# Optimization experiments

Hardware: AMD Instinct MI355X
Metric: run time of the kernel (lower is better)

The kernel has to match this reference:

```python
import jax, jax.numpy as jnp
import numpy as np

H = 8          # nhead
EPS_Z = 1e-6   # linear-attention normalizer eps
LN_EPS = 1e-5  # torch LayerNorm default


def _ln(x, g, b):
    m = x.mean(-1, keepdims=True)
    v = ((x - m) ** 2).mean(-1, keepdims=True)
    return (x - m) * jax.lax.rsqrt(v + LN_EPS) * g + b


def setup_inputs() -> dict:
    key = jax.random.key(0)
    ks = jax.random.split(key, 8)
    B, S, E, F = 4, 8192, 512, 2048
    s = 0.02
    return {
        "src": jax.random.normal(ks[0], (B, S, E), jnp.float32),
        "Wq": jax.random.normal(ks[1], (E, E), jnp.float32) * s,
        "bq": jnp.zeros((E,), jnp.float32),
        "Wk": jax.random.normal(ks[2], (E, E), jnp.float32) * s,
        "bk": jnp.zeros((E,), jnp.float32),
        "Wv": jax.random.normal(ks[3], (E, E), jnp.float32) * s,
        "bv": jnp.zeros((E,), jnp.float32),
        "Wo": jax.random.normal(ks[4], (E, E), jnp.float32) * s,
        "bo": jnp.zeros((E,), jnp.float32),
        "W1": jax.random.normal(ks[5], (E, F), jnp.float32) * s,
        "b1": jnp.zeros((F,), jnp.float32),
        "W2": jax.random.normal(ks[6], (F, E), jnp.float32) * s,
        "b2": jnp.zeros((E,), jnp.float32),
        "g1": jnp.ones((E,), jnp.float32),
        "be1": jnp.zeros((E,), jnp.float32),
        "g2": jnp.ones((E,), jnp.float32),
        "be2": jnp.zeros((E,), jnp.float32),
    }


def reference(src, Wq, bq, Wk, bk, Wv, bv, Wo, bo, W1, b1, W2, b2, g1, be1, g2, be2):
    B, S, E = src.shape
    Dh = E // H

    def heads(x):  # [B,S,E] -> [B,H,S,Dh]
        return x.reshape(B, S, H, Dh).transpose(0, 2, 1, 3)

    q = heads(src @ Wq + bq)
    k = heads(src @ Wk + bk)
    v = heads(src @ Wv + bv)

    qm = jax.nn.elu(q) + 1.0  # feature map: ELU+1
    km = jax.nn.elu(k) + 1.0

    kv = jnp.einsum("bhsd,bhse->bhde", km, v)          # [B,H,Dh,Dh]
    ksum = km.sum(axis=2)                               # [B,H,Dh]
    z = 1.0 / (jnp.einsum("bhsd,bhd->bhs", qm, ksum) + EPS_Z)
    attn = jnp.einsum("bhsd,bhde->bhse", qm, kv) * z[..., None]

    attn = attn.transpose(0, 2, 1, 3).reshape(B, S, E) @ Wo + bo
    x = _ln(src + attn, g1, be1)
    ff = jax.nn.relu(x @ W1 + b1) @ W2 + b2
    return _ln(x + ff, g2, be2)
```

## Files before the change

kernel.cpp:

```cpp
#include <hip/hip_runtime.h>
#include <hip/hip_bf16.h>

typedef __attribute__((ext_vector_type(8))) short bf16x8;
typedef __attribute__((ext_vector_type(4))) float f32x4;

__device__ inline ushort f2bf(float f) {
    uint u = __float_as_uint(f);
    u += 0x7fff + ((u >> 16) & 1);
    return (ushort)(u >> 16);
}
__device__ inline float bf2f(ushort h) {
    return __uint_as_float(((uint)h) << 16);
}

__device__ inline void gload16(const void* g, void* lds) {
    __builtin_amdgcn_global_load_lds(
        (const __attribute__((address_space(1))) void*)g,
        (__attribute__((address_space(3))) void*)lds, 16, 0, 0);
}

__global__ __launch_bounds__(256) void prep(
    const float* __restrict__ src, ushort* __restrict__ src16,
    const float* __restrict__ Wq, const float* __restrict__ Wk,
    const float* __restrict__ Wv, const float* __restrict__ Wo,
    const float* __restrict__ W1, const float* __restrict__ W2,
    ushort* __restrict__ wqkv, ushort* __restrict__ wot,
    ushort* __restrict__ w1t, ushort* __restrict__ w2t,
    const float* __restrict__ bq, const float* __restrict__ bk,
    const float* __restrict__ bv, float* __restrict__ bqkv) {
    __shared__ float tile[32][33];
    int bid = blockIdx.x;
    const int t = threadIdx.x;
    if (bid < 16384) {
        int i = bid * 256 + t;
        float4 a = ((const float4*)src)[i];
        ushort4 o;
        o.x = f2bf(a.x); o.y = f2bf(a.y); o.z = f2bf(a.z); o.w = f2bf(a.w);
        ((ushort4*)src16)[i] = o;
        return;
    }
    bid -= 16384;
    const float* in; ushort* out; int Kd, Nd;
    if (bid < 1024) {
        int m = bid >> 8;
        in = (m == 0) ? Wq : (m == 1) ? Wk : (m == 2) ? Wv : Wo;
        out = (m == 3) ? wot : (wqkv + m * 512 * 512);
        Kd = 512; Nd = 512; bid &= 255;
    } else if (bid < 2048) { in = W1; out = w1t; Kd = 512; Nd = 2048; bid -= 1024; }
    else if (bid < 3072) { in = W2; out = w2t; Kd = 2048; Nd = 512; bid -= 2048; }
    else {
        int i = (bid - 3072) * 256 + t;
        if (i < 512) bqkv[i] = bq[i];
        else if (i < 1024) bqkv[i] = bk[i - 512];
        else if (i < 1536) bqkv[i] = bv[i - 1024];
        return;
    }
    const int nx = Nd / 32;
    const int nbase = (bid % nx) * 32, kb = (bid / nx) * 32;
    const int tx = t & 31, ty = t >> 5;
#pragma unroll
    for (int i = 0; i < 4; i++)
        tile[ty + i * 8][tx] = in[(size_t)(kb + ty + i * 8) * Nd + nbase + tx];
    __syncthreads();
#pragma unroll
    for (int i = 0; i < 4; i++) {
        int n = nbase + ty + i * 8, k = kb + tx;
        out[(size_t)n * Kd + k] = f2bf(tile[tx][ty + i * 8]);
    }
}

template <int EPI, int NT, int GB>
__global__ __launch_bounds__(512, 2) void gemm256(
    const ushort* __restrict__ A, const ushort* __restrict__ Bt,
    const float* __restrict__ bias, const ushort* __restrict__ res16,
    ushort* __restrict__ out16, int M, int N, int K, int nb1) {
    extern __shared__ char smem[];
    const int t = threadIdx.x;
    const int w = t >> 6, l = t & 63;
    const int wr = w >> 2, wc = w & 3;
    const int nwg = gridDim.x;
    const int cpx = nwg >> 3;
    const int swz = (blockIdx.x & 7) * cpx + (blockIdx.x >> 3);
    int bx0, by0;
    if (GB == 0) { bx0 = (swz % nb1) * NT; by0 = swz / nb1; }
    else         { bx0 = swz % nb1;        by0 = (swz / nb1) * NT; }

    const int sc = (t & 3) ^ ((t >> 3) & 3);
    const ushort* gA0 = A + (size_t)(by0 * 256 + (t >> 2)) * K + sc * 8;
    const ushort* gA1 = gA0 + (size_t)128 * K;
    const ushort* gB0 = Bt + (size_t)(bx0 * 256 + (t >> 2)) * K + sc * 8;
    const ushort* gB1 = gB0 + (size_t)128 * K;

    const int Kt = K >> 5;
    const int TOT = NT * Kt;
    int stg_kt = 0, stg_g = 0;
    size_t stgA = 0, stgB = 0;

    auto stage_h0 = [&]() {
        char* Lb = smem + (stg_g & 3) * 32768 + (w << 10);
        gload16(gA0 + stgA + stg_kt * 32, Lb);
        gload16(gB0 + stgB + stg_kt * 32, Lb + 16384);
    };
    auto stage_h1 = [&]() {
        char* Lb = smem + (stg_g & 3) * 32768 + (w << 10);
        gload16(gA1 + stgA + stg_kt * 32, Lb + 8192);
        gload16(gB1 + stgB + stg_kt * 32, Lb + 24576);
        ++stg_g;
        if (++stg_kt == Kt) {
            stg_kt = 0;
            if (GB == 0) stgB += (size_t)256 * K;
            else         stgA += (size_t)256 * K;
        }
    };

    f32x4 acc[8][4] = {};

    const int R0a = wr * 128 + (l & 15);
    const int offA = R0a * 64 + (((l >> 4) ^ ((R0a >> 1) & 3)) << 4);
    const int R0b = wc * 64 + (l & 15);
    const int offB = 16384 + R0b * 64 + (((l >> 4) ^ ((R0b >> 1) & 3)) << 4);

    stage_h0(); stage_h1();
    stage_h0(); stage_h1();
    stage_h0(); stage_h1();

    int g = 0;
    for (int j = 0; j < NT; ++j) {
#pragma unroll 1
        for (int kt = 0; kt < Kt; ++kt, ++g) {
            const int rem = TOT - 1 - g;
            if (rem >= 2)      asm volatile("s_waitcnt vmcnt(8)" ::: "memory");
            else if (rem == 1) asm volatile("s_waitcnt vmcnt(4)" ::: "memory");
            else               asm volatile("s_waitcnt vmcnt(0)" ::: "memory");
            __builtin_amdgcn_s_barrier();
            __builtin_amdgcn_sched_barrier(0);

            const char* bufp = smem + (g & 3) * 32768;
            if (g + 3 < TOT) { stage_h0(); stage_h1(); }

            bf16x8 a[8], b[4];
#pragma unroll
            for (int n = 0; n < 4; n++) b[n] = *(const bf16x8*)(bufp + offB + n * 1024);
#pragma unroll
            for (int m = 0; m < 8; m++) a[m] = *(const bf16x8*)(bufp + offA + m * 1024);

            __builtin_amdgcn_s_setprio(1);
#pragma unroll
            for (int m = 0; m < 8; m++)
#pragma unroll
                for (int n = 0; n < 4; n++)
                    acc[m][n] = __builtin_amdgcn_mfma_f32_16x16x32_bf16(a[m], b[n], acc[m][n], 0, 0, 0);
            __builtin_amdgcn_s_setprio(0);
            __builtin_amdgcn_sched_barrier(0);
        }

        {
            const int bx = (GB == 0) ? (bx0 + j) : bx0;
            const int by = (GB == 0) ? by0 : (by0 + j);
            const int row0 = by * 256 + wr * 128 + ((l >> 4) << 2);
            const int col0 = bx * 256 + wc * 64 + (l & 15);
            const int seg = bx >> 1;
            const size_t segoff = (size_t)seg * M * 512;
            const int c511 = col0 & 511;
            float bv[4];
#pragma unroll
            for (int n = 0; n < 4; n++) bv[n] = bias[col0 + n * 16];
#pragma unroll
            for (int m = 0; m < 8; m++) {
#pragma unroll
                for (int r = 0; r < 4; r++) {
                    const int row = row0 + m * 16 + r;
                    const size_t base = (size_t)row * N + col0;
#pragma unroll
                    for (int n = 0; n < 4; n++) {
                        float vv = acc[m][n][r] + bv[n];
                        if constexpr (EPI == 2) {
                            vv = vv > 0.f ? vv : 0.f;
                            out16[base + n * 16] = f2bf(vv);
                        } else if constexpr (EPI == 3) {
                            vv += bf2f(res16[base + n * 16]);
                            out16[base + n * 16] = f2bf(vv);
                        } else if constexpr (EPI == 4) {
                            if (seg < 2) vv = vv > 0.f ? vv + 1.f : __expf(vv);
                            out16[segoff + (size_t)row * 512 + c511 + n * 16] = f2bf(vv);
                        } else {
                            out16[base + n * 16] = f2bf(vv);
                        }
                    }
                }
            }
            if (j + 1 < NT) {
#pragma unroll
                for (int m = 0; m < 8; m++)
#pragma unroll
                    for (int n = 0; n < 4; n++)
                        acc[m][n] = (f32x4){0.f, 0.f, 0.f, 0.f};
            }
        }
    }
}

__global__ __launch_bounds__(256) void kv_partial(
    const ushort* __restrict__ km, const ushort* __restrict__ v,
    float* __restrict__ kvp, float* __restrict__ ksump, int S) {
    __shared__ ushort kms[32 * 64];
    __shared__ ushort vs[32 * 64];
    const int t = threadIdx.x;
    const int bh = blockIdx.y, b = bh >> 3, h = bh & 7;
    const int d0 = (t >> 4) * 4, e0 = (t & 15) * 4;
    float acc[4][4] = {};
    float ks = 0.f;
    const int s_base = blockIdx.x * 512;
    const int r = t >> 3, c8 = (t & 7) * 8;
    for (int s0 = 0; s0 < 512; s0 += 32) {
        size_t grow = ((size_t)b * S + s_base + s0 + r) * 512 + h * 64 + c8;
        *(uint4*)&kms[r * 64 + c8] = *(const uint4*)&km[grow];
        *(uint4*)&vs[r * 64 + c8] = *(const uint4*)&v[grow];
        __syncthreads();
#pragma unroll 4
        for (int s = 0; s < 32; ++s) {
            ushort4 ka = *(const ushort4*)&kms[s * 64 + d0];
            ushort4 vb = *(const ushort4*)&vs[s * 64 + e0];
            float a0 = bf2f(ka.x), a1 = bf2f(ka.y), a2 = bf2f(ka.z), a3 = bf2f(ka.w);
            float b0 = bf2f(vb.x), b1 = bf2f(vb.y), b2 = bf2f(vb.z), b3 = bf2f(vb.w);
            acc[0][0] += a0 * b0; acc[0][1] += a0 * b1; acc[0][2] += a0 * b2; acc[0][3] += a0 * b3;
            acc[1][0] += a1 * b0; acc[1][1] += a1 * b1; acc[1][2] += a1 * b2; acc[1][3] += a1 * b3;
            acc[2][0] += a2 * b0; acc[2][1] += a2 * b1; acc[2][2] += a2 * b2; acc[2][3] += a2 * b3;
            acc[3][0] += a3 * b0; acc[3][1] += a3 * b1; acc[3][2] += a3 * b2; acc[3][3] += a3 * b3;
            if (t < 64) ks += bf2f(kms[s * 64 + t]);
        }
        __syncthreads();
    }
    float* dst = kvp + ((size_t)bh * 16 + blockIdx.x) * 4096;
#pragma unroll
    for (int i = 0; i < 4; i++)
#pragma unroll
        for (int j = 0; j < 4; j++)
            dst[(d0 + i) * 64 + e0 + j] = acc[i][j];
    if (t < 64) ksump[((size_t)bh * 16 + blockIdx.x) * 64 + t] = ks;
}

__global__ void kv_reduce(const float* __restrict__ kvp, const float* __restrict__ ksump,
                          ushort* __restrict__ kvt, float* __restrict__ ksum) {
    int i = blockIdx.x * 256 + threadIdx.x;
    if (i < 32 * 4096) {
        int bh = i >> 12, de = i & 4095;
        int d = de >> 6, e = de & 63;
        float s = 0.f;
#pragma unroll
        for (int c = 0; c < 16; ++c) s += kvp[((size_t)bh * 16 + c) * 4096 + de];
        kvt[(size_t)bh * 4096 + e * 64 + d] = f2bf(s);
    } else {
        int j = i - 32 * 4096;
        if (j < 32 * 64) {
            int bh = j >> 6, d = j & 63;
            float s = 0.f;
#pragma unroll
            for (int c = 0; c < 16; ++c) s += ksump[((size_t)bh * 16 + c) * 64 + d];
            ksum[j] = s;
        }
    }
}

__global__ __launch_bounds__(256) void attn_mfma(
    const ushort* __restrict__ qm, const ushort* __restrict__ kvt,
    const float* __restrict__ ksum, ushort* __restrict__ attnE, int S) {
    __shared__ ushort As[128 * 128];
    __shared__ ushort Bs[128 * 64];
    __shared__ float zbuf[128][2];
    __shared__ float ks2[128];
    const int t = threadIdx.x, w = t >> 6, l = t & 63;
    const int cx = blockIdx.x, by = blockIdx.y;
    const int b = (by * 128) / S;
    const int h0 = cx * 2;
    const size_t arow0 = (size_t)(by * 128) * 512 + cx * 128;

#pragma unroll
    for (int rd = 0; rd < 8; ++rd) {
        const ushort* g = qm + arow0 + (size_t)(rd * 16 + w * 4 + (l >> 4)) * 512 + (l & 15) * 8;
        gload16(g, (char*)As + rd * 4096 + w * 1024);
    }
    const ushort* kvbase = kvt + (size_t)(b * 8 + h0) * 4096;
#pragma unroll
    for (int rd = 0; rd < 4; ++rd) {
        const ushort* g = kvbase + (rd * 32 + w * 8 + (l >> 3)) * 64 + (l & 7) * 8;
        gload16(g, (char*)Bs + rd * 4096 + w * 1024);
    }
    if (t < 128) ks2[t] = ksum[(b * 8 + h0) * 64 + t];
    __syncthreads();

    {
        const int r = t >> 1, hh = t & 1;
        float den = 0.f;
#pragma unroll
        for (int d0 = 0; d0 < 64; d0 += 8) {
            bf16x8 qv = *(const bf16x8*)&As[r * 128 + hh * 64 + d0];
#pragma unroll
            for (int j = 0; j < 8; j++) den += bf2f((ushort)qv[j]) * ks2[hh * 64 + d0 + j];
        }
        zbuf[r][hh] = 1.0f / (den + 1e-6f);
    }

    const int wr = w >> 1, wc = w & 1;
    const int ar = wr * 64 + (l & 15);
    const int br = wc * 64 + (l & 15);
    const int ko = (l >> 4) * 8;
    f32x4 acc[4][4] = {};
#pragma unroll
    for (int ks_ = 0; ks_ < 2; ++ks_) {
        bf16x8 a[4], bb[4];
#pragma unroll
        for (int m = 0; m < 4; m++)
            a[m] = *(const bf16x8*)&As[(ar + m * 16) * 128 + wc * 64 + ks_ * 32 + ko];
#pragma unroll
        for (int n = 0; n < 4; n++)
            bb[n] = *(const bf16x8*)&Bs[(br + n * 16) * 64 + ks_ * 32 + ko];
#pragma unroll
        for (int m = 0; m < 4; m++)
#pragma unroll
            for (int n = 0; n < 4; n++)
                acc[m][n] = __builtin_amdgcn_mfma_f32_16x16x32_bf16(a[m], bb[n], acc[m][n], 0, 0, 0);
    }
    __syncthreads();

    const int row0l = wr * 64 + ((l >> 4) << 2);
    ushort* outbase = attnE + (size_t)(by * 128) * 512 + cx * 128;
#pragma unroll
    for (int n = 0; n < 4; n++) {
#pragma unroll
        for (int m = 0; m < 4; m++) {
#pragma unroll
            for (int r = 0; r < 4; r++) {
                int rl = row0l + m * 16 + r;
                float z = zbuf[rl][wc];
                outbase[(size_t)rl * 512 + wc * 64 + n * 16 + (l & 15)] = f2bf(acc[m][n][r] * z);
            }
        }
    }
}

template <int OUT32>
__global__ __launch_bounds__(256) void ln_bf16(
    const ushort* __restrict__ in, const float* __restrict__ g, const float* __restrict__ be,
    void* __restrict__ outp, int Mrows) {
    const int w = threadIdx.x >> 6, l = threadIdx.x & 63;
    const int row = blockIdx.x * 4 + w;
    if (row >= Mrows) return;
    const ushort* rp = in + (size_t)row * 512;
    uint4 u = *(const uint4*)&rp[l * 8];
    float x[8];
    x[0] = bf2f((ushort)(u.x & 0xffff)); x[1] = bf2f((ushort)(u.x >> 16));
    x[2] = bf2f((ushort)(u.y & 0xffff)); x[3] = bf2f((ushort)(u.y >> 16));
    x[4] = bf2f((ushort)(u.z & 0xffff)); x[5] = bf2f((ushort)(u.z >> 16));
    x[6] = bf2f((ushort)(u.w & 0xffff)); x[7] = bf2f((ushort)(u.w >> 16));
    float s = 0.f, ss = 0.f;
#pragma unroll
    for (int j = 0; j < 8; j++) { s += x[j]; ss += x[j] * x[j]; }
#pragma unroll
    for (int o = 1; o < 64; o <<= 1) {
        s += __shfl_xor(s, o, 64);
        ss += __shfl_xor(ss, o, 64);
    }
    float mean = s * (1.f / 512.f);
    float var = ss * (1.f / 512.f) - mean * mean;
    float rstd = rsqrtf(var + 1e-5f);
    float4 g0 = *(const float4*)&g[l * 8], g1v = *(const float4*)&g[l * 8 + 4];
    float4 b0 = *(const float4*)&be[l * 8], b1v = *(const float4*)&be[l * 8 + 4];
    float o0[8];
    o0[0] = (x[0] - mean) * rstd * g0.x + b0.x;
    o0[1] = (x[1] - mean) * rstd * g0.y + b0.y;
    o0[2] = (x[2] - mean) * rstd * g0.z + b0.z;
    o0[3] = (x[3] - mean) * rstd * g0.w + b0.w;
    o0[4] = (x[4] - mean) * rstd * g1v.x + b1v.x;
    o0[5] = (x[5] - mean) * rstd * g1v.y + b1v.y;
    o0[6] = (x[6] - mean) * rstd * g1v.z + b1v.z;
    o0[7] = (x[7] - mean) * rstd * g1v.w + b1v.w;
    if constexpr (OUT32) {
        float* op = (float*)outp + (size_t)row * 512;
        *(float4*)&op[l * 8] = make_float4(o0[0], o0[1], o0[2], o0[3]);
        *(float4*)&op[l * 8 + 4] = make_float4(o0[4], o0[5], o0[6], o0[7]);
    } else {
        ushort* op = (ushort*)outp + (size_t)row * 512;
        ushort4 u0, u1;
        u0.x = f2bf(o0[0]); u0.y = f2bf(o0[1]); u0.z = f2bf(o0[2]); u0.w = f2bf(o0[3]);
        u1.x = f2bf(o0[4]); u1.y = f2bf(o0[5]); u1.z = f2bf(o0[6]); u1.w = f2bf(o0[7]);
        *(ushort4*)&op[l * 8] = u0;
        *(ushort4*)&op[l * 8 + 4] = u1;
    }
}

extern "C" void kernel_launch(void* const* d_in, const int* in_sizes, int n_in,
                              void* d_out, int out_size, void* d_ws, size_t ws_size,
                              hipStream_t stream) {
    const int B = 4, S = 8192, E = 512, F = 2048;
    const int M = B * S;
    const size_t SZ = (size_t)M * E * 2;
    const int SMEM = 131072;

    const float* src = (const float*)d_in[0];
    const float* Wq = (const float*)d_in[1];  const float* bq = (const float*)d_in[2];
    const float* Wk = (const float*)d_in[3];  const float* bk = (const float*)d_in[4];
    const float* Wv = (const float*)d_in[5];  const float* bv = (const float*)d_in[6];
    const float* Wo = (const float*)d_in[7];  const float* bo = (const float*)d_in[8];
    const float* W1 = (const float*)d_in[9];  const float* b1 = (const float*)d_in[10];
    const float* W2 = (const float*)d_in[11]; const float* b2 = (const float*)d_in[12];
    const float* g1 = (const float*)d_in[13]; const float* be1 = (const float*)d_in[14];
    const float* g2 = (const float*)d_in[15]; const float* be2 = (const float*)d_in[16];

    char* ws = (char*)d_ws;
    ushort* qm    = (ushort*)(ws + 0 * SZ);
    ushort* km    = (ushort*)(ws + 1 * SZ);
    ushort* v     = (ushort*)(ws + 2 * SZ);
    ushort* src16 = (ushort*)(ws + 3 * SZ);
    ushort* x16   = (ushort*)(ws + 4 * SZ);
    ushort* z16   = (ushort*)(ws + 5 * SZ);
    char*   tail  = ws + 6 * SZ;
    float*  kvp   = (float*)(tail);
    float*  ksump = (float*)(tail + 8388608);
    ushort* kvt   = (ushort*)(tail + 8519680);
    float*  ksum  = (float*)(tail + 8781824);
    float*  bqkv  = (float*)(tail + 8790016);
    ushort* wqkv  = (ushort*)(tail + 8796160);
    ushort* wot   = (ushort*)(tail + 10369024);
    ushort* w1t   = (ushort*)(tail + 10893312);
    ushort* w2t   = (ushort*)(tail + 12990464);
    ushort* attnE = km;
    ushort* y16   = v;
    ushort* hbuf  = (ushort*)(ws + 0);

    hipFuncSetAttribute((const void*)gemm256<4, 3, 0>, hipFuncAttributeMaxDynamicSharedMemorySize, SMEM);
    hipFuncSetAttribute((const void*)gemm256<3, 1, 0>, hipFuncAttributeMaxDynamicSharedMemorySize, SMEM);
    hipFuncSetAttribute((const void*)gemm256<2, 4, 1>, hipFuncAttributeMaxDynamicSharedMemorySize, SMEM);

    prep<<<dim3(16384 + 3072 + 6), 256, 0, stream>>>(
        src, src16, Wq, Wk, Wv, Wo, W1, W2, wqkv, wot, w1t, w2t, bq, bk, bv, bqkv);

    gemm256<4, 3, 0><<<dim3(2 * 128), 512, SMEM, stream>>>(src16, wqkv, bqkv, nullptr, qm, M, 1536, E, 2);

    kv_partial<<<dim3(16, 32), 256, 0, stream>>>(km, v, kvp, ksump, S);
    kv_reduce<<<dim3((32 * 4096 + 32 * 64 + 255) / 256), 256, 0, stream>>>(kvp, ksump, kvt, ksum);

    attn_mfma<<<dim3(4, M / 128), 256, 0, stream>>>(qm, kvt, ksum, attnE, S);

    gemm256<3, 1, 0><<<dim3(2 * 128), 512, SMEM, stream>>>(attnE, wot, bo, src16, y16, M, E, E, 2);
    ln_bf16<0><<<dim3(M / 4), 256, 0, stream>>>(y16, g1, be1, x16, M);

    gemm256<2, 4, 1><<<dim3(8 * 32), 512, SMEM, stream>>>(x16, w1t, b1, nullptr, hbuf, M, F, E, 8);
    gemm256<3, 1, 0><<<dim3(2 * 128), 512, SMEM, stream>>>(hbuf, w2t, b2, x16, z16, M, E, F, 2);
    ln_bf16<1><<<dim3(M / 4), 256, 0, stream>>>(z16, g2, be2, (float*)d_out, M);
}
```

Measured before the change: 364.8 us.

## Restructure GEMM mainloop to double-buffered BK=64 with interleaved staging phases

The 256x256 bf16 GEMM drops its 4-stage BK=32 ring buffer for a 2-stage BK=64 double buffer with an 8-way XOR swizzle. Each K-step is split into four phases that interleave LDS fragment reads, global-to-LDS staging of the next tile, fine-grained vmcnt/lgkmcnt waits and MFMA groups, with barriers between phases. The goal is to halve loop overhead per K and overlap loads with compute more evenly. In exchange there are many more barriers per iteration and a shallower prefetch depth, which could expose memory latency.

```diff
diff --git a/kernel.cpp b/kernel.cpp
--- a/kernel.cpp
+++ b/kernel.cpp
@@ -78,80 +78,103 @@
     const int t = threadIdx.x;
     const int w = t >> 6, l = t & 63;
     const int wr = w >> 2, wc = w & 3;
-    const int nwg = gridDim.x;
-    const int cpx = nwg >> 3;
+    const int nwg = gridDim.x, cpx = nwg >> 3;
     const int swz = (blockIdx.x & 7) * cpx + (blockIdx.x >> 3);
     int bx0, by0;
     if (GB == 0) { bx0 = (swz % nb1) * NT; by0 = swz / nb1; }
     else         { bx0 = swz % nb1;        by0 = (swz / nb1) * NT; }
 
-    const int sc = (t & 3) ^ ((t >> 3) & 3);
-    const ushort* gA0 = A + (size_t)(by0 * 256 + (t >> 2)) * K + sc * 8;
-    const ushort* gA1 = gA0 + (size_t)128 * K;
-    const ushort* gB0 = Bt + (size_t)(bx0 * 256 + (t >> 2)) * K + sc * 8;
-    const ushort* gB1 = gB0 + (size_t)128 * K;
-
-    const int Kt = K >> 5;
+    const int scoff = ((t & 7) ^ ((t >> 3) & 7)) * 8;
+    const ushort* pA = A + (size_t)(by0 * 256 + (t >> 3)) * K + scoff;
+    const ushort* pB = Bt + (size_t)(bx0 * 256 + (t >> 3)) * K + scoff;
+    const size_t u64K = (size_t)64 * K;
+
+    const int Kt = K >> 6;
     const int TOT = NT * Kt;
-    int stg_kt = 0, stg_g = 0;
-    size_t stgA = 0, stgB = 0;
-
-    auto stage_h0 = [&]() {
-        char* Lb = smem + (stg_g & 3) * 32768 + (w << 10);
-        gload16(gA0 + stgA + stg_kt * 32, Lb);
-        gload16(gB0 + stgB + stg_kt * 32, Lb + 16384);
-    };
-    auto stage_h1 = [&]() {
-        char* Lb = smem + (stg_g & 3) * 32768 + (w << 10);
-        gload16(gA1 + stgA + stg_kt * 32, Lb + 8192);
-        gload16(gB1 + stgB + stg_kt * 32, Lb + 24576);
-        ++stg_g;
-        if (++stg_kt == Kt) {
-            stg_kt = 0;
-            if (GB == 0) stgB += (size_t)256 * K;
-            else         stgA += (size_t)256 * K;
-        }
-    };
+    int skt = 0;
+    size_t adv = 0;
+
+    const int cA0 = ((l >> 4) ^ (l & 7)) * 16;
+    const int cA1 = ((4 + (l >> 4)) ^ (l & 7)) * 16;
+    const int baseA = (wr * 128 + (l & 15)) * 128;
+    const int baseB = 32768 + (wc * 64 + (l & 15)) * 128;
+
+    char* nb = smem;
+
+#define STG(uid)                                                                        \
+    {                                                                                   \
+        char* dst = nb + ((uid) < 4 ? (uid) * 8192 : 32768 + ((uid) - 4) * 8192) + (w << 10); \
+        const ushort* s = ((uid) < 4)                                                   \
+            ? (pA + (size_t)(uid) * u64K + (GB ? adv : 0) + skt * 64)                   \
+            : (pB + (size_t)((uid) - 4) * u64K + (GB ? 0 : adv) + skt * 64);            \
+        gload16(s, dst);                                                                \
+    }
+
+    STG(4); STG(5); STG(6); STG(7); STG(0); STG(2); STG(1); STG(3);
+    if (++skt == Kt) { skt = 0; adv += (size_t)256 * K; }
+    asm volatile("s_waitcnt vmcnt(2)" ::: "memory");
+    __builtin_amdgcn_s_barrier();
 
     f32x4 acc[8][4] = {};
-
-    const int R0a = wr * 128 + (l & 15);
-    const int offA = R0a * 64 + (((l >> 4) ^ ((R0a >> 1) & 3)) << 4);
-    const int R0b = wc * 64 + (l & 15);
-    const int offB = 16384 + R0b * 64 + (((l >> 4) ^ ((R0b >> 1) & 3)) << 4);
-
-    stage_h0(); stage_h1();
-    stage_h0(); stage_h1();
-    stage_h0(); stage_h1();
-
+    bf16x8 b[4][2];
     int g = 0;
     for (int j = 0; j < NT; ++j) {
 #pragma unroll 1
         for (int kt = 0; kt < Kt; ++kt, ++g) {
-            const int rem = TOT - 1 - g;
-            if (rem >= 2)      asm volatile("s_waitcnt vmcnt(8)" ::: "memory");
-            else if (rem == 1) asm volatile("s_waitcnt vmcnt(4)" ::: "memory");
-            else               asm volatile("s_waitcnt vmcnt(0)" ::: "memory");
-            __builtin_amdgcn_s_barrier();
-            __builtin_amdgcn_sched_barrier(0);
-
-            const char* bufp = smem + (g & 3) * 32768;
-            if (g + 3 < TOT) { stage_h0(); stage_h1(); }
-
-            bf16x8 a[8], b[4];
-#pragma unroll
-            for (int n = 0; n < 4; n++) b[n] = *(const bf16x8*)(bufp + offB + n * 1024);
-#pragma unroll
-            for (int m = 0; m < 8; m++) a[m] = *(const bf16x8*)(bufp + offA + m * 1024);
-
-            __builtin_amdgcn_s_setprio(1);
-#pragma unroll
-            for (int m = 0; m < 8; m++)
-#pragma unroll
-                for (int n = 0; n < 4; n++)
-                    acc[m][n] = __builtin_amdgcn_mfma_f32_16x16x32_bf16(a[m], b[n], acc[m][n], 0, 0, 0);
-            __builtin_amdgcn_s_setprio(0);
-            __builtin_amdgcn_sched_barrier(0);
+            const char* cb = smem + (g & 1) * 65536;
+            nb = smem + ((g + 1) & 1) * 65536;
+            const bool ds = (g + 1 < TOT);
+#pragma unroll
+            for (int p = 0; p < 4; ++p) {
+                bf16x8 af[2][2];
+                if (p == 0) {
+#pragma unroll
+                    for (int n = 0; n < 4; n++) {
+                        b[n][0] = *(const bf16x8*)(cb + baseB + n * 2048 + cA0);
+                        b[n][1] = *(const bf16x8*)(cb + baseB + n * 2048 + cA1);
+                    }
+                }
+                af[0][0] = *(const bf16x8*)(cb + baseA + (2 * p) * 2048 + cA0);
+                af[0][1] = *(const bf16x8*)(cb + baseA + (2 * p) * 2048 + cA1);
+                af[1][0] = *(const bf16x8*)(cb + baseA + (2 * p + 1) * 2048 + cA0);
+                af[1][1] = *(const bf16x8*)(cb + baseA + (2 * p + 1) * 2048 + cA1);
+                if (ds) {
+                    if (p == 0)      { STG(4); STG(5); }
+                    else if (p == 1) { STG(6); STG(7); }
+                    else if (p == 2) { STG(0); STG(2); }
+                    else             { STG(1); STG(3); }
+                }
+                if (p == 0) asm volatile("s_waitcnt lgkmcnt(8)" ::: "memory");
+                if (p == 1) {
+                    if (ds) asm volatile("s_waitcnt vmcnt(4)" ::: "memory");
+                    else    asm volatile("s_waitcnt vmcnt(0)" ::: "memory");
+                }
+                if (p == 3) {
+                    if (ds) asm volatile("s_waitcnt vmcnt(2)" ::: "memory");
+                    else    asm volatile("s_waitcnt vmcnt(0)" ::: "memory");
+                }
+                __builtin_amdgcn_sched_barrier(0);
+                __builtin_amdgcn_s_barrier();
+                asm volatile("s_waitcnt lgkmcnt(0)" ::: "memory");
+                __builtin_amdgcn_sched_barrier(0);
+                __builtin_amdgcn_s_setprio(1);
+#pragma unroll
+                for (int i = 0; i < 2; i++)
+#pragma unroll
+                    for (int n = 0; n < 4; n++) {
+                        acc[2 * p + i][n] = __builtin_amdgcn_mfma_f32_16x16x32_bf16(
+                            af[i][0], b[n][0], acc[2 * p + i][n], 0, 0, 0);
+                        acc[2 * p + i][n] = __builtin_amdgcn_mfma_f32_16x16x32_bf16(
+                            af[i][1], b[n][1], acc[2 * p + i][n], 0, 0, 0);
+                    }
+                __builtin_amdgcn_s_setprio(0);
+                __builtin_amdgcn_sched_barrier(0);
+                __builtin_amdgcn_s_barrier();
+                __builtin_amdgcn_sched_barrier(0);
+            }
+            if (ds) {
+                if (++skt == Kt) { skt = 0; adv += (size_t)256 * K; }
+            }
         }
 
         {
@@ -198,6 +221,7 @@
             }
         }
     }
+#undef STG
 }
 
 __global__ __launch_bounds__(256) void kv_partial(
```

Result: slower. 376.3 us (+3.2%).

## Switch GEMM to BK=64 double-buffered LDS pipeline with vmcnt(0) waits

Applied to the files above, without the earlier changes.

The GEMM main loop now stages K tiles of 64 instead of 32, using two 64KB LDS buffers instead of four 32KB ring buffers. The XOR swizzle is widened to 8 chunks of 16 bytes to match, and each iteration issues two MFMA passes per tile. Prefetch depth drops from three tiles ahead to one, with a full vmcnt(0) wait each step, and the s_setprio hints are removed. This halves the number of barriers per K, but it exposes more global-load latency and uses 128KB of LDS per block, which may limit occupancy.

```diff
diff --git a/kernel.cpp b/kernel.cpp
--- a/kernel.cpp
+++ b/kernel.cpp
@@ -78,80 +78,73 @@
     const int t = threadIdx.x;
     const int w = t >> 6, l = t & 63;
     const int wr = w >> 2, wc = w & 3;
-    const int nwg = gridDim.x;
-    const int cpx = nwg >> 3;
+    const int nwg = gridDim.x, cpx = nwg >> 3;
     const int swz = (blockIdx.x & 7) * cpx + (blockIdx.x >> 3);
     int bx0, by0;
     if (GB == 0) { bx0 = (swz % nb1) * NT; by0 = swz / nb1; }
     else         { bx0 = swz % nb1;        by0 = (swz / nb1) * NT; }
 
-    const int sc = (t & 3) ^ ((t >> 3) & 3);
-    const ushort* gA0 = A + (size_t)(by0 * 256 + (t >> 2)) * K + sc * 8;
-    const ushort* gA1 = gA0 + (size_t)128 * K;
-    const ushort* gB0 = Bt + (size_t)(bx0 * 256 + (t >> 2)) * K + sc * 8;
-    const ushort* gB1 = gB0 + (size_t)128 * K;
-
-    const int Kt = K >> 5;
+    const int scoff = ((t & 7) ^ ((t >> 3) & 7)) * 8;
+    const ushort* pA = A + (size_t)(by0 * 256 + (t >> 3)) * K + scoff;
+    const ushort* pB = Bt + (size_t)(bx0 * 256 + (t >> 3)) * K + scoff;
+    const size_t u64K = (size_t)64 * K;
+
+    const int Kt = K >> 6;
     const int TOT = NT * Kt;
-    int stg_kt = 0, stg_g = 0;
-    size_t stgA = 0, stgB = 0;
-
-    auto stage_h0 = [&]() {
-        char* Lb = smem + (stg_g & 3) * 32768 + (w << 10);
-        gload16(gA0 + stgA + stg_kt * 32, Lb);
-        gload16(gB0 + stgB + stg_kt * 32, Lb + 16384);
-    };
-    auto stage_h1 = [&]() {
-        char* Lb = smem + (stg_g & 3) * 32768 + (w << 10);
-        gload16(gA1 + stgA + stg_kt * 32, Lb + 8192);
-        gload16(gB1 + stgB + stg_kt * 32, Lb + 24576);
-        ++stg_g;
-        if (++stg_kt == Kt) {
-            stg_kt = 0;
-            if (GB == 0) stgB += (size_t)256 * K;
-            else         stgA += (size_t)256 * K;
-        }
-    };
+    int skt = 0;
+    size_t adv = 0;
+
+#define STG8(buf)                                                              \
+    {                                                                          \
+        char* Lb = (buf) + (w << 10);                                          \
+        _Pragma("unroll")                                                      \
+        for (int u = 0; u < 4; ++u) {                                          \
+            gload16(pA + (size_t)u * u64K + (GB ? adv : 0) + skt * 64,         \
+                    Lb + u * 8192);                                            \
+            gload16(pB + (size_t)u * u64K + (GB ? 0 : adv) + skt * 64,         \
+                    Lb + 32768 + u * 8192);                                    \
+        }                                                                      \
+        if (++skt == Kt) { skt = 0; adv += (size_t)256 * K; }                  \
+    }
+
+    const int cA0 = ((l >> 4) ^ (l & 7)) * 16;
+    const int cA1 = ((4 + (l >> 4)) ^ (l & 7)) * 16;
+    const int baseA = (wr * 128 + (l & 15)) * 128;
+    const int baseB = 32768 + (wc * 64 + (l & 15)) * 128;
+
+    STG8(smem);
 
     f32x4 acc[8][4] = {};
-
-    const int R0a = wr * 128 + (l & 15);
-    const int offA = R0a * 64 + (((l >> 4) ^ ((R0a >> 1) & 3)) << 4);
-    const int R0b = wc * 64 + (l & 15);
-    const int offB = 16384 + R0b * 64 + (((l >> 4) ^ ((R0b >> 1) & 3)) << 4);
-
-    stage_h0(); stage_h1();
-    stage_h0(); stage_h1();
-    stage_h0(); stage_h1();
-
     int g = 0;
     for (int j = 0; j < NT; ++j) {
 #pragma unroll 1
         for (int kt = 0; kt < Kt; ++kt, ++g) {
-            const int rem = TOT - 1 - g;
-            if (rem >= 2)      asm volatile("s_waitcnt vmcnt(8)" ::: "memory");
-            else if (rem == 1) asm volatile("s_waitcnt vmcnt(4)" ::: "memory");
-            else               asm volatile("s_waitcnt vmcnt(0)" ::: "memory");
+            asm volatile("s_waitcnt vmcnt(0)" ::: "memory");
             __builtin_amdgcn_s_barrier();
             __builtin_amdgcn_sched_barrier(0);
 
-            const char* bufp = smem + (g & 3) * 32768;
-            if (g + 3 < TOT) { stage_h0(); stage_h1(); }
+            const char* cb = smem + (g & 1) * 65536;
+            if (g + 1 < TOT) STG8(smem + ((g + 1) & 1) * 65536);
 
             bf16x8 a[8], b[4];
 #pragma unroll
-            for (int n = 0; n < 4; n++) b[n] = *(const bf16x8*)(bufp + offB + n * 1024);
-#pragma unroll
-            for (int m = 0; m < 8; m++) a[m] = *(const bf16x8*)(bufp + offA + m * 1024);
-
-            __builtin_amdgcn_s_setprio(1);
+            for (int n = 0; n < 4; n++) b[n] = *(const bf16x8*)(cb + baseB + n * 2048 + cA0);
+#pragma unroll
+            for (int m = 0; m < 8; m++) a[m] = *(const bf16x8*)(cb + baseA + m * 2048 + cA0);
 #pragma unroll
             for (int m = 0; m < 8; m++)
 #pragma unroll
                 for (int n = 0; n < 4; n++)
                     acc[m][n] = __builtin_amdgcn_mfma_f32_16x16x32_bf16(a[m], b[n], acc[m][n], 0, 0, 0);
-            __builtin_amdgcn_s_setprio(0);
-            __builtin_amdgcn_sched_barrier(0);
+#pragma unroll
+            for (int n = 0; n < 4; n++) b[n] = *(const bf16x8*)(cb + baseB + n * 2048 + cA1);
+#pragma unroll
+            for (int m = 0; m < 8; m++) a[m] = *(const bf16x8*)(cb + baseA + m * 2048 + cA1);
+#pragma unroll
+            for (int m = 0; m < 8; m++)
+#pragma unroll
+                for (int n = 0; n < 4; n++)
+                    acc[m][n] = __builtin_amdgcn_mfma_f32_16x16x32_bf16(a[m], b[n], acc[m][n], 0, 0, 0);
         }
 
         {
@@ -198,6 +191,7 @@
             }
         }
     }
+#undef STG8
 }
 
 __global__ __launch_bounds__(256) void kv_partial(
```

Measured after the change: 357.5 us. 1.02x faster.
